# Kernel optimization log

Measured on AMD Instinct MI355X. Metric: run time of the kernel, lower is better.

The kernel has to match this reference:

```python
import jax, jax.numpy as jnp
import numpy as np
from jax import lax


def _lstm_seq(x, W, U, b):
    """Keras-style LSTM over full sequence. x: [B,T,D] -> hs: [B,T,H].
    Gate order i, f, c(g), o; zero initial state; sigmoid/tanh activations."""
    B, T, D = x.shape
    H = U.shape[0]
    # Precompute input projection for all timesteps (one big GEMM).
    xz = jnp.einsum('btd,dg->btg', x, W) + b  # [B,T,4H]

    def step(carry, xz_t):
        h, c = carry
        z = xz_t + h @ U  # [B,4H]
        i, f, g, o = jnp.split(z, 4, axis=-1)
        i = jax.nn.sigmoid(i)
        f = jax.nn.sigmoid(f)
        g = jnp.tanh(g)
        o = jax.nn.sigmoid(o)
        c = f * c + i * g
        h = o * jnp.tanh(c)
        return (h, c), h

    h0 = jnp.zeros((B, H), dtype=x.dtype)
    c0 = jnp.zeros((B, H), dtype=x.dtype)
    (_, _), hs = lax.scan(step, (h0, c0), jnp.swapaxes(xz, 0, 1))  # hs: [T,B,H]
    return jnp.swapaxes(hs, 0, 1)  # [B,T,H]


def setup_inputs() -> dict:
    key = jax.random.key(0)
    ks = jax.random.split(key, 7)
    B, T, D, H = 64, 256, 1024, 1024
    s = 0.05  # weight scale to keep gates out of saturation
    x = jax.random.normal(ks[0], (B, T, 1, D), dtype=jnp.float32)
    Wf = jax.random.normal(ks[1], (D, 4 * H), dtype=jnp.float32) * s
    Uf = jax.random.normal(ks[2], (H, 4 * H), dtype=jnp.float32) * s
    bf = jnp.zeros((4 * H,), dtype=jnp.float32)
    Wb = jax.random.normal(ks[3], (D, 4 * H), dtype=jnp.float32) * s
    Ub = jax.random.normal(ks[4], (H, 4 * H), dtype=jnp.float32) * s
    bb = jnp.zeros((4 * H,), dtype=jnp.float32)
    return {"x": x, "Wf": Wf, "Uf": Uf, "bf": bf, "Wb": Wb, "Ub": Ub, "bb": bb}


def reference(x, Wf, Uf, bf, Wb, Ub, bb):
    # call(): squeeze axis=2, BiLSTM (concat), flatten. training=False -> dropout off.
    xs = jnp.squeeze(x, axis=2)  # [B,T,D]
    h_fwd = _lstm_seq(xs, Wf, Uf, bf)  # [B,T,H]
    # go_backwards=True: process reversed sequence; Bidirectional re-reverses output.
    h_bwd = _lstm_seq(xs[:, ::-1, :], Wb, Ub, bb)[:, ::-1, :]  # [B,T,H]
    out = jnp.concatenate([h_fwd, h_bwd], axis=-1)  # [B,T,2H]
    B = out.shape[0]
    return out.reshape(B, -1)  # Flatten -> [B, T*2H]
```

## Files before the change

### kernel.cpp

```cpp
#include <hip/hip_runtime.h>
#include <hip/hip_bf16.h>

typedef unsigned short u16;
typedef unsigned long long u64;
typedef short short8 __attribute__((ext_vector_type(8)));
typedef float floatx4 __attribute__((ext_vector_type(4)));

#define BATCH 64
#define SEQT  256
#define DDIM  1024
#define HDIM  1024
#define GDIM  4096
#define MROWS 16384
#define BH    (BATCH * HDIM)

__device__ __forceinline__ u16 f2bf(float f) {
  unsigned u = __builtin_bit_cast(unsigned, f);
  u += 0x7fffu + ((u >> 16) & 1u);
  return (u16)(u >> 16);
}
__device__ __forceinline__ float bf2f(u16 v) {
  unsigned u = ((unsigned)v) << 16;
  return __builtin_bit_cast(float, u);
}
__device__ __forceinline__ float xz2f(float v) { return v; }
__device__ __forceinline__ float xz2f(u16 v) { return bf2f(v); }

template <typename T> __device__ __forceinline__ T f2xz(float v);
template <> __device__ __forceinline__ float f2xz<float>(float v) { return v; }
template <> __device__ __forceinline__ u16 f2xz<u16>(float v) { return f2bf(v); }

__device__ __forceinline__ float sigm(float x) { return 1.0f / (1.0f + __expf(-x)); }
__device__ __forceinline__ float tanh_(float x) {
  float a = __expf(2.0f * fabsf(x));
  float r = 1.0f - 2.0f / (a + 1.0f);
  return x >= 0.0f ? r : -r;
}

__device__ __forceinline__ void async16(const void* g, void* l) {
  __builtin_amdgcn_global_load_lds(
      (const __attribute__((address_space(1))) unsigned int*)g,
      (__attribute__((address_space(3))) unsigned int*)l, 16, 0, 0);
}

__device__ __forceinline__ void st_agent(unsigned* p, unsigned v) {
  __hip_atomic_store(p, v, __ATOMIC_RELAXED, __HIP_MEMORY_SCOPE_AGENT);
}

__device__ __forceinline__ void grid_barrier(unsigned* bar_, int wdg, int l, unsigned epoch) {
  __syncthreads();
  if (threadIdx.x == 0)
    __hip_atomic_store(bar_ + wdg, epoch, __ATOMIC_RELAXED, __HIP_MEMORY_SCOPE_AGENT);
  if (threadIdx.x < 64) {
    unsigned a, b;
    do {
      __builtin_amdgcn_s_sleep(2);
      a = __hip_atomic_load(bar_ + l,      __ATOMIC_RELAXED, __HIP_MEMORY_SCOPE_AGENT);
      b = __hip_atomic_load(bar_ + 64 + l, __ATOMIC_RELAXED, __HIP_MEMORY_SCOPE_AGENT);
    } while (!__all(a >= epoch && b >= epoch));
  }
  __syncthreads();
}

__global__ __launch_bounds__(256) void k_cvt_x(const float* __restrict__ in,
                                               u16* __restrict__ out) {
  long i = ((long)blockIdx.x * 256 + threadIdx.x) * 4;
  float4 v = *(const float4*)(in + i);
  u16 o0 = f2bf(v.x), o1 = f2bf(v.y), o2 = f2bf(v.z), o3 = f2bf(v.w);
  unsigned lo = (unsigned)o0 | ((unsigned)o1 << 16);
  unsigned hi = (unsigned)o2 | ((unsigned)o3 << 16);
  uint2 p; p.x = lo; p.y = hi;
  *(uint2*)(out + i) = p;
}

__global__ __launch_bounds__(256) void k_tc(const float* __restrict__ S0, const float* __restrict__ S1,
                                            const float* __restrict__ S2, const float* __restrict__ S3,
                                            u16* __restrict__ D0, u16* __restrict__ D1,
                                            u16* __restrict__ D2, u16* __restrict__ D3) {
  const float* src; u16* dst;
  switch (blockIdx.z) {
    case 0: src = S0; dst = D0; break;
    case 1: src = S1; dst = D1; break;
    case 2: src = S2; dst = D2; break;
    default: src = S3; dst = D3; break;
  }
  __shared__ __align__(16) float tl[64][65];
  const int k0 = blockIdx.x * 64, n0 = blockIdx.y * 64;
  const int tid = threadIdx.x, col = tid & 63, rq = tid >> 6;
#pragma unroll
  for (int i = 0; i < 16; i++) {
    int r = i * 4 + rq;
    tl[r][col] = src[(long)(k0 + r) * GDIM + n0 + col];
  }
  __syncthreads();
#pragma unroll
  for (int i = 0; i < 16; i++) {
    int r = i * 4 + rq;
    dst[(long)(n0 + r) * DDIM + k0 + col] = f2bf(tl[col][r]);
  }
}

template <typename XZT>
__global__ __launch_bounds__(256) void k_gemm(const u16* __restrict__ A,
                                              const u16* __restrict__ BtF, const u16* __restrict__ BtB,
                                              const float* __restrict__ biasF, const float* __restrict__ biasB,
                                              XZT* __restrict__ xzF, XZT* __restrict__ xzB) {
  const u16* Bt = blockIdx.z ? BtB : BtF;
  const float* bias = blockIdx.z ? biasB : biasF;
  XZT* xz = blockIdx.z ? xzB : xzF;
  const int m0 = blockIdx.x * 128, n0 = blockIdx.y * 128;
  __shared__ __align__(16) u16 Al[128 * 32];
  __shared__ __align__(16) u16 Bl[128 * 32];
  const int tid = threadIdx.x, w = tid >> 6, l = tid & 63;
  const int wm = w & 1, wn = w >> 1;
  floatx4 acc[4][4];
#pragma unroll
  for (int i = 0; i < 4; i++)
#pragma unroll
    for (int j = 0; j < 4; j++) acc[i][j] = (floatx4)(0.0f);

  const int srow = w * 32 + (l >> 2);
  const char* Ag = (const char*)(A + (long)(m0 + srow) * DDIM) + (l & 3) * 16;
  const char* Bg = (const char*)(Bt + (long)(n0 + srow) * DDIM) + (l & 3) * 16;
  char* Asl = (char*)Al + w * 2048;
  char* Bsl = (char*)Bl + w * 2048;

  for (int kt = 0; kt < 32; kt++) {
    __syncthreads();
    async16(Ag, Asl);
    async16(Ag + 16 * 2048, Asl + 1024);
    async16(Bg, Bsl);
    async16(Bg + 16 * 2048, Bsl + 1024);
    Ag += 64; Bg += 64;
    __syncthreads();
    short8 af[4], bfr[4];
#pragma unroll
    for (int i = 0; i < 4; i++) {
      af[i]  = *(const short8*)(Al + (wm * 64 + i * 16 + (l & 15)) * 32 + (l >> 4) * 8);
      bfr[i] = *(const short8*)(Bl + (wn * 64 + i * 16 + (l & 15)) * 32 + (l >> 4) * 8);
    }
#pragma unroll
    for (int i = 0; i < 4; i++)
#pragma unroll
      for (int j = 0; j < 4; j++)
        acc[i][j] = __builtin_amdgcn_mfma_f32_16x16x32_bf16(af[i], bfr[j], acc[i][j], 0, 0, 0);
  }
  const int c = l & 15, q = l >> 4;
#pragma unroll
  for (int j = 0; j < 4; j++) {
    const int n = n0 + wn * 64 + j * 16 + c;
    const float bv = bias[n];
#pragma unroll
    for (int i = 0; i < 4; i++) {
      const long mb = (long)(m0 + wm * 64 + i * 16 + q * 4);
#pragma unroll
      for (int r = 0; r < 4; r++)
        xz[(mb + r) * GDIM + n] = f2xz<XZT>(acc[i][j][r] + bv);
    }
  }
}

template <typename XZT>
__global__ __launch_bounds__(512, 2) void k_lstm(const XZT* __restrict__ xzF, const XZT* __restrict__ xzB,
                                                 const u16* __restrict__ UtF, const u16* __restrict__ UtB,
                                                 u16* __restrict__ hbuf, float* __restrict__ out,
                                                 unsigned* __restrict__ bar) {
  extern __shared__ __align__(16) char lds[];
  char* hlb = lds;
  float* zl = (float*)lds;

  const int wg = blockIdx.x;
  const int dir = wg >> 6;
  const int wd = wg & 63;
  const int j0 = wd * 16;
  const int tid = threadIdx.x;
  const int wv = tid >> 6, l = tid & 63;
  const int c = l & 15, q = l >> 4;
  const int g = wv & 3, rh = wv >> 2;
  const u16* Ut = dir ? UtB : UtF;
  const XZT* xz = dir ? xzB : xzF;
  u16* hb = hbuf + (size_t)dir * (4 * BH);

  const int ucol = g * 1024 + j0 + c;
  short8 uf[32];
#pragma unroll
  for (int kt = 0; kt < 32; kt++)
    uf[kt] = *(const short8*)(Ut + (long)ucol * DDIM + kt * 32 + q * 8);

  const int eb = tid >> 3;
  const int jj = (tid & 7) * 2;
  {
    u16* hz = hb + eb * HDIM + j0 + jj;
    st_agent((unsigned*)hz, 0u);
    st_agent((unsigned*)(hz + BH), 0u);
  }
  float cs0 = 0.0f, cs1 = 0.0f;

  float xv0[4], xv1[4];
  auto prefetch = [&](int s) {
    const int t = dir ? (SEQT - 1 - s) : s;
#pragma unroll
    for (int r = 0; r < 4; r++) {
      xv0[r] = xz2f(xz[((long)(rh * 32 + q * 4 + r)      * SEQT + t) * GDIM + ucol]);
      xv1[r] = xz2f(xz[((long)(rh * 32 + 16 + q * 4 + r) * SEQT + t) * GDIM + ucol]);
    }
  };
  prefetch(0);

  const unsigned swz = ((unsigned)(c & 7)) << 4;
  const unsigned qo = (unsigned)(q * 16);
  const unsigned rbase0 = (unsigned)((rh * 32 + c) * 2048);
  const unsigned rbase1 = rbase0 + 16 * 2048;

  const unsigned rot = (unsigned)(wd * 2048);

  for (int s = 0; s < SEQT; s++) {
    grid_barrier(bar, dir * 64 + wd, l, (unsigned)(s + 1));
    const int p = s & 1;
    const int t = dir ? (SEQT - 1 - s) : s;

    const u64 sbase = (u64)(hb + (size_t)(2 * p + (wd & 1)) * BH);
    short8 sv[16];
    unsigned sb[16];
#pragma unroll
    for (int j = 0; j < 16; j++) {
      sb[j] = ((unsigned)(tid * 16 + j * 8192) + rot) & 131071u;
      asm volatile("global_load_dwordx4 %0, %1, %2 sc0 sc1"
                   : "=v"(sv[j]) : "v"(sb[j]), "s"(sbase));
    }
#pragma unroll
    for (int j = 0; j < 16; j++) {
      asm volatile("s_waitcnt vmcnt(%1)" : "+v"(sv[j]) : "n"(15 - j));
      const unsigned sw = sb[j] ^ ((sb[j] >> 7) & 0x70u);
      *(short8*)(hlb + sw) = sv[j];
    }
    __syncthreads();

    floatx4 a0 = (floatx4)(0.0f), a1 = (floatx4)(0.0f);
#pragma unroll
    for (int kt = 0; kt < 32; kt++) {
      const unsigned off = (((unsigned)(kt * 64)) | qo) ^ swz;
      short8 af0 = *(const short8*)(hlb + rbase0 + off);
      short8 af1 = *(const short8*)(hlb + rbase1 + off);
      a0 = __builtin_amdgcn_mfma_f32_16x16x32_bf16(af0, uf[kt], a0, 0, 0, 0);
      a1 = __builtin_amdgcn_mfma_f32_16x16x32_bf16(af1, uf[kt], a1, 0, 0, 0);
    }
    __syncthreads();

#pragma unroll
    for (int r = 0; r < 4; r++) {
      zl[(rh * 32 + q * 4 + r) * 68 + g * 16 + c]      = a0[r] + xv0[r];
      zl[(rh * 32 + 16 + q * 4 + r) * 68 + g * 16 + c] = a1[r] + xv1[r];
    }
    __syncthreads();

    const float* zrow = zl + eb * 68;
    float zi0 = zrow[jj],      zi1 = zrow[jj + 1];
    float zf0 = zrow[16 + jj], zf1 = zrow[16 + jj + 1];
    float zg0 = zrow[32 + jj], zg1 = zrow[32 + jj + 1];
    float zo0 = zrow[48 + jj], zo1 = zrow[48 + jj + 1];
    float i0 = sigm(zi0), f0 = sigm(zf0), g0 = tanh_(zg0), o0 = sigm(zo0);
    float i1 = sigm(zi1), f1 = sigm(zf1), g1 = tanh_(zg1), o1 = sigm(zo1);
    cs0 = f0 * cs0 + i0 * g0;
    cs1 = f1 * cs1 + i1 * g1;
    float h0v = o0 * tanh_(cs0), h1v = o1 * tanh_(cs1);

    unsigned hpair = (unsigned)f2bf(h0v) | ((unsigned)f2bf(h1v) << 16);
    u16* hw = hb + (size_t)(2 * (1 - p)) * BH + eb * HDIM + j0 + jj;
    st_agent((unsigned*)hw, hpair);
    st_agent((unsigned*)(hw + BH), hpair);
    *(float2*)(out + (long)eb * (SEQT * 2 * HDIM) + (long)t * (2 * HDIM) + dir * HDIM + j0 + jj)
        = make_float2(h0v, h1v);

    if (s + 1 < SEQT) prefetch(s + 1);
  }
}

extern "C" void kernel_launch(void* const* d_in, const int* in_sizes, int n_in,
                              void* d_out, int out_size, void* d_ws, size_t ws_size,
                              hipStream_t stream) {
  const float* x   = (const float*)d_in[0];
  const float* Wf  = (const float*)d_in[1];
  const float* Uf  = (const float*)d_in[2];
  const float* bf_ = (const float*)d_in[3];
  const float* Wb  = (const float*)d_in[4];
  const float* Ub  = (const float*)d_in[5];
  const float* bb  = (const float*)d_in[6];
  float* out = (float*)d_out;
  char* ws = (char*)d_ws;

  const size_t SZ_XBF = (size_t)MROWS * DDIM * 2;
  const size_t SZ_WT  = (size_t)GDIM * DDIM * 2;
  const size_t SZ_H   = (size_t)2 * 4 * BH * 2;

  size_t off = 2048;
  u16* xbf = (u16*)(ws + off); off += SZ_XBF;
  u16* WtF = (u16*)(ws + off); off += SZ_WT;
  u16* WtB = (u16*)(ws + off); off += SZ_WT;
  u16* UtF = (u16*)(ws + off); off += SZ_WT;
  u16* UtB = (u16*)(ws + off); off += SZ_WT;
  u16* hb  = (u16*)(ws + off); off += SZ_H;
  size_t xz_off = (off + 1023) & ~(size_t)1023;

  const size_t XZ_F32 = (size_t)MROWS * GDIM * 4;
  const size_t XZ_BF  = (size_t)MROWS * GDIM * 2;
  const bool fp32xz = ws_size >= xz_off + 2 * XZ_F32;

  unsigned* bar = (unsigned*)ws;
  hipMemsetAsync(bar, 0, 2048, stream);
  k_cvt_x<<<MROWS * DDIM / 1024, 256, 0, stream>>>(x, xbf);
  k_tc<<<dim3(16, 64, 4), 256, 0, stream>>>(Wf, Uf, Wb, Ub, WtF, UtF, WtB, UtB);

  if (fp32xz) {
    float* xzF = (float*)(ws + xz_off);
    float* xzB = (float*)(ws + xz_off + XZ_F32);
    k_gemm<float><<<dim3(128, 32, 2), 256, 0, stream>>>(xbf, WtF, WtB, bf_, bb, xzF, xzB);
    hipFuncSetAttribute((const void*)k_lstm<float>,
                        hipFuncAttributeMaxDynamicSharedMemorySize, 131072);
    k_lstm<float><<<128, 512, 131072, stream>>>(xzF, xzB, UtF, UtB, hb, out, bar);
  } else {
    u16* xzF = (u16*)(ws + xz_off);
    u16* xzB = (u16*)(ws + xz_off + XZ_BF);
    k_gemm<u16><<<dim3(128, 32, 2), 256, 0, stream>>>(xbf, WtF, WtB, bf_, bb, xzF, xzB);
    hipFuncSetAttribute((const void*)k_lstm<u16>,
                        hipFuncAttributeMaxDynamicSharedMemorySize, 131072);
    k_lstm<u16><<<128, 512, 131072, stream>>>(xzF, xzB, UtF, UtB, hb, out, bar);
  }
}
```

Before: 3.556 ms.

## Use per-step hidden-state history with async global-to-LDS loads

Replaces the double-buffered, duplicated hidden-state buffers with a full per-timestep history array, so each step reads a fresh buffer and writes only one copy. The h staging now uses async16 direct global-to-LDS copies with the swizzle moved to the source address, instead of register loads followed by LDS stores. This is meant to cut the duplicate stores, the load-wait-store latency and the register pressure on the recurrent critical path. In exchange it uses more workspace, drops the per-workgroup rotation that spread reads across copies, and relies on fresh addresses rather than sc0/sc1 cache bypass for coherence.

```diff
diff --git a/kernel.cpp b/kernel.cpp
--- a/kernel.cpp
+++ b/kernel.cpp
@@ -163,7 +163,7 @@
 template <typename XZT>
 __global__ __launch_bounds__(512, 2) void k_lstm(const XZT* __restrict__ xzF, const XZT* __restrict__ xzB,
                                                  const u16* __restrict__ UtF, const u16* __restrict__ UtB,
-                                                 u16* __restrict__ hbuf, float* __restrict__ out,
+                                                 u16* __restrict__ hist, float* __restrict__ out,
                                                  unsigned* __restrict__ bar) {
   extern __shared__ __align__(16) char lds[];
   char* hlb = lds;
@@ -179,7 +179,7 @@
   const int g = wv & 3, rh = wv >> 2;
   const u16* Ut = dir ? UtB : UtF;
   const XZT* xz = dir ? xzB : xzF;
-  u16* hb = hbuf + (size_t)dir * (4 * BH);
+  u16* hd = hist + (size_t)dir * ((SEQT + 1) * (size_t)BH);
 
   const int ucol = g * 1024 + j0 + c;
   short8 uf[32];
@@ -189,11 +189,7 @@
 
   const int eb = tid >> 3;
   const int jj = (tid & 7) * 2;
-  {
-    u16* hz = hb + eb * HDIM + j0 + jj;
-    st_agent((unsigned*)hz, 0u);
-    st_agent((unsigned*)(hz + BH), 0u);
-  }
+  st_agent((unsigned*)(hd + eb * HDIM + j0 + jj), 0u);
   float cs0 = 0.0f, cs1 = 0.0f;
 
   float xv0[4], xv1[4];
@@ -212,27 +208,16 @@
   const unsigned rbase0 = (unsigned)((rh * 32 + c) * 2048);
   const unsigned rbase1 = rbase0 + 16 * 2048;
 
-  const unsigned rot = (unsigned)(wd * 2048);
-
   for (int s = 0; s < SEQT; s++) {
     grid_barrier(bar, dir * 64 + wd, l, (unsigned)(s + 1));
-    const int p = s & 1;
     const int t = dir ? (SEQT - 1 - s) : s;
 
-    const u64 sbase = (u64)(hb + (size_t)(2 * p + (wd & 1)) * BH);
-    short8 sv[16];
-    unsigned sb[16];
+    const char* hsrc = (const char*)(hd + (size_t)s * BH);
 #pragma unroll
     for (int j = 0; j < 16; j++) {
-      sb[j] = ((unsigned)(tid * 16 + j * 8192) + rot) & 131071u;
-      asm volatile("global_load_dwordx4 %0, %1, %2 sc0 sc1"
-                   : "=v"(sv[j]) : "v"(sb[j]), "s"(sbase));
-    }
-#pragma unroll
-    for (int j = 0; j < 16; j++) {
-      asm volatile("s_waitcnt vmcnt(%1)" : "+v"(sv[j]) : "n"(15 - j));
-      const unsigned sw = sb[j] ^ ((sb[j] >> 7) & 0x70u);
-      *(short8*)(hlb + sw) = sv[j];
+      const unsigned lin = (unsigned)(tid * 16 + j * 8192);
+      const unsigned src = lin ^ ((lin >> 7) & 0x70u);
+      async16(hsrc + src, hlb + (unsigned)(wv * 1024 + j * 8192));
     }
     __syncthreads();
 
@@ -266,9 +251,7 @@
     float h0v = o0 * tanh_(cs0), h1v = o1 * tanh_(cs1);
 
     unsigned hpair = (unsigned)f2bf(h0v) | ((unsigned)f2bf(h1v) << 16);
-    u16* hw = hb + (size_t)(2 * (1 - p)) * BH + eb * HDIM + j0 + jj;
-    st_agent((unsigned*)hw, hpair);
-    st_agent((unsigned*)(hw + BH), hpair);
+    st_agent((unsigned*)(hd + (size_t)(s + 1) * BH + eb * HDIM + j0 + jj), hpair);
     *(float2*)(out + (long)eb * (SEQT * 2 * HDIM) + (long)t * (2 * HDIM) + dir * HDIM + j0 + jj)
         = make_float2(h0v, h1v);
 
@@ -289,17 +272,17 @@
   float* out = (float*)d_out;
   char* ws = (char*)d_ws;
 
-  const size_t SZ_XBF = (size_t)MROWS * DDIM * 2;
-  const size_t SZ_WT  = (size_t)GDIM * DDIM * 2;
-  const size_t SZ_H   = (size_t)2 * 4 * BH * 2;
+  const size_t SZ_XBF  = (size_t)MROWS * DDIM * 2;
+  const size_t SZ_WT   = (size_t)GDIM * DDIM * 2;
+  const size_t SZ_HIST = (size_t)2 * (SEQT + 1) * BH * 2;
 
   size_t off = 2048;
-  u16* xbf = (u16*)(ws + off); off += SZ_XBF;
-  u16* WtF = (u16*)(ws + off); off += SZ_WT;
-  u16* WtB = (u16*)(ws + off); off += SZ_WT;
-  u16* UtF = (u16*)(ws + off); off += SZ_WT;
-  u16* UtB = (u16*)(ws + off); off += SZ_WT;
-  u16* hb  = (u16*)(ws + off); off += SZ_H;
+  u16* xbf  = (u16*)(ws + off); off += SZ_XBF;
+  u16* WtF  = (u16*)(ws + off); off += SZ_WT;
+  u16* WtB  = (u16*)(ws + off); off += SZ_WT;
+  u16* UtF  = (u16*)(ws + off); off += SZ_WT;
+  u16* UtB  = (u16*)(ws + off); off += SZ_WT;
+  u16* hist = (u16*)(ws + off); off += SZ_HIST;
   size_t xz_off = (off + 1023) & ~(size_t)1023;
 
   const size_t XZ_F32 = (size_t)MROWS * GDIM * 4;
@@ -317,13 +300,13 @@
     k_gemm<float><<<dim3(128, 32, 2), 256, 0, stream>>>(xbf, WtF, WtB, bf_, bb, xzF, xzB);
     hipFuncSetAttribute((const void*)k_lstm<float>,
                         hipFuncAttributeMaxDynamicSharedMemorySize, 131072);
-    k_lstm<float><<<128, 512, 131072, stream>>>(xzF, xzB, UtF, UtB, hb, out, bar);
+    k_lstm<float><<<128, 512, 131072, stream>>>(xzF, xzB, UtF, UtB, hist, out, bar);
   } else {
     u16* xzF = (u16*)(ws + xz_off);
     u16* xzB = (u16*)(ws + xz_off + XZ_BF);
     k_gemm<u16><<<dim3(128, 32, 2), 256, 0, stream>>>(xbf, WtF, WtB, bf_, bb, xzF, xzB);
     hipFuncSetAttribute((const void*)k_lstm<u16>,
                         hipFuncAttributeMaxDynamicSharedMemorySize, 131072);
-    k_lstm<u16><<<128, 512, 131072, stream>>>(xzF, xzB, UtF, UtB, hb, out, bar);
-  }
-}
+    k_lstm<u16><<<128, 512, 131072, stream>>>(xzF, xzB, UtF, UtB, hist, out, bar);
+  }
+}
```

Result: faster. 3.022 ms (-15.0%).
